# Optimization experiments

Hardware: AMD Instinct MI355X
Metric: run time of the kernel (lower is better)

Reference implementation:

```python
import jax, jax.numpy as jnp
import numpy as np

EPS = 1e-5

def _rmsnorm(x):
    # BitLinear applies a (non-learnable) RMSNorm to activations before quantization
    return x * jax.lax.rsqrt(jnp.mean(x * x, axis=-1, keepdims=True) + EPS)

def _activation_quant(x):
    # per-token absmax int8 quantization, dequantized back to float
    scale = 127.0 / jnp.clip(jnp.max(jnp.abs(x), axis=-1, keepdims=True), EPS, None)
    return jnp.clip(jnp.round(x * scale), -128, 127) / scale

def _weight_quant(w):
    # absmean ternary {-1,0,1} quantization, dequantized back to float
    scale = 1.0 / jnp.clip(jnp.mean(jnp.abs(w)), EPS, None)
    return jnp.clip(jnp.round(w * scale), -1, 1) / scale

def _bitlinear(x, w):
    xn = _rmsnorm(x)
    # straight-through estimators (identity grads through quantizers)
    xq = xn + jax.lax.stop_gradient(_activation_quant(xn) - xn)
    wq = w + jax.lax.stop_gradient(_weight_quant(w) - w)
    return jnp.einsum('bsd,hd->bsh', xq, wq)

def setup_inputs() -> dict:
    key = jax.random.key(0)
    k1, k2, k3, k4 = jax.random.split(key, 4)
    B, S, D, H = 4, 2048, 4096, 11008
    return {
        'x': jax.random.normal(k1, (B, S, D), dtype=jnp.float32),
        'w_gate': jax.random.normal(k2, (H, D), dtype=jnp.float32) * 0.02,
        'w_up': jax.random.normal(k3, (H, D), dtype=jnp.float32) * 0.02,
        'w_down': jax.random.normal(k4, (D, H), dtype=jnp.float32) * 0.02,
    }

def reference(x, w_gate, w_up, w_down):
    h = jax.nn.silu(_bitlinear(x, w_gate)) * _bitlinear(x, w_up)
    return _bitlinear(h, w_down)
```

## Files before the change

### kernel.cpp

```cpp
#include <hip/hip_runtime.h>
#include <hip/hip_bf16.h>
#include <cstdint>

#define EPS 1e-5

typedef __attribute__((ext_vector_type(4))) int int32x4;


__device__ inline float np_leaf_abs(const float* __restrict__ a, int n) {
  float r[8];
  #pragma unroll
  for (int j = 0; j < 8; j++) r[j] = fabsf(a[j]);
  for (int i = 8; i < n; i += 8) {
    #pragma unroll
    for (int j = 0; j < 8; j++) r[j] += fabsf(a[i + j]);
  }
  return ((r[0] + r[1]) + (r[2] + r[3])) + ((r[4] + r[5]) + (r[6] + r[7]));
}

__global__ __launch_bounds__(256) void np_blocksums3(
    const float* __restrict__ w0, const float* __restrict__ w1,
    const float* __restrict__ w2, float* __restrict__ bs) {
  int b = blockIdx.x * 256 + threadIdx.x;
  const float* w = (b < 131072) ? w0 : (b < 262144 ? w1 : w2);
  long lb = b & 131071;
  const float* a = w + lb * 344;
  float s0 = np_leaf_abs(a, 80);
  float s1 = np_leaf_abs(a + 80, 88);
  float s2 = np_leaf_abs(a + 168, 88);
  float s3 = np_leaf_abs(a + 256, 88);
  bs[b] = (s0 + s1) + (s2 + s3);
}

__global__ __launch_bounds__(256) void np_tree_partial3(
    const float* __restrict__ bs, float* __restrict__ part) {
  __shared__ float sh[256];
  int t = threadIdx.x;
  const float* a = bs + (long)blockIdx.x * 512;
  sh[t] = a[2 * t] + a[2 * t + 1];
  __syncthreads();
  for (int n = 128; n >= 1; n >>= 1) {
    float x = 0.f;
    if (t < n) x = sh[2 * t] + sh[2 * t + 1];
    __syncthreads();
    if (t < n) sh[t] = x;
    __syncthreads();
  }
  if (t == 0) part[blockIdx.x] = sh[0];
}

__global__ __launch_bounds__(128) void np_tree_final3(
    const float* __restrict__ part, float* __restrict__ meanw) {
  __shared__ float sh[128];
  int t = threadIdx.x;
  const float* p = part + blockIdx.x * 256;
  sh[t] = p[2 * t] + p[2 * t + 1];
  __syncthreads();
  for (int n = 64; n >= 1; n >>= 1) {
    float x = 0.f;
    if (t < n) x = sh[2 * t] + sh[2 * t + 1];
    __syncthreads();
    if (t < n) sh[t] = x;
    __syncthreads();
  }
  if (t == 0) meanw[blockIdx.x] = sh[0] / 45088768.0f;
}

__global__ __launch_bounds__(256) void quant_w_gu(
    const float* __restrict__ wg, const float* __restrict__ wu,
    const float* __restrict__ meanw, char* __restrict__ qg, char* __restrict__ qu,
    long n4) {
  int half = (blockIdx.x >= 4096);
  const float* w = half ? wu : wg;
  char* q = half ? qu : qg;
  float scale = 1.0f / fmaxf(meanw[half], 1e-5f);
  long i = (long)(blockIdx.x & 4095) * blockDim.x + threadIdx.x;
  long stride = 4096L * blockDim.x;
  const float4* w4 = (const float4*)w;
  for (; i < n4; i += stride) {
    float4 v = w4[i];
    char4 c;
    c.x = (char)(int)fminf(1.f, fmaxf(-1.f, rintf(v.x * scale)));
    c.y = (char)(int)fminf(1.f, fmaxf(-1.f, rintf(v.y * scale)));
    c.z = (char)(int)fminf(1.f, fmaxf(-1.f, rintf(v.z * scale)));
    c.w = (char)(int)fminf(1.f, fmaxf(-1.f, rintf(v.w * scale)));
    long row = i >> 10;
    int  col = (int)(i & 1023) << 2;
    long p = row >> 4; int rl = (int)(row & 15);
    int  cc = col >> 6, s = (col >> 4) & 3, j = col & 15;
    *(char4*)(q + ((p * 64 + cc) * 64 + (s << 4) + rl) * 16 + j) = c;
  }
}

#define CORR_MAX 1024
#define WIN 1e-6f

__global__ __launch_bounds__(256) void quant_w_down(
    const float* __restrict__ w, const float* __restrict__ mean_ptr,
    char* __restrict__ q, int* __restrict__ cnt,
    int* __restrict__ ck, float* __restrict__ cv) {
  float scale = 1.0f / fmaxf(mean_ptr[2], 1e-5f);
  long i0 = (long)blockIdx.x * blockDim.x + threadIdx.x;
  long stride = (long)gridDim.x * blockDim.x;
  const long ncell = 4096L * 2752L;
  for (long i = i0; i < ncell; i += stride) {
    long row = i / 2752;
    int  col = (int)(i - row * 2752) << 2;
    const float* wp = w + row * 11008 + col;
    char4 c;
    #pragma unroll
    for (int j = 0; j < 4; j++) {
      float t = wp[j] * scale;
      float qv = fminf(1.f, fmaxf(-1.f, rintf(t)));
      if (fabsf(fabsf(t) - 0.5f) < WIN) {
        qv = 0.f;
        int idx = atomicAdd(cnt, 1);
        if (idx < CORR_MAX) {
          ck[idx] = (int)(row * 11008 + col + j);
          cv[idx] = t > 0.f ? 0.5f : -0.5f;
        }
      }
      ((char*)&c)[j] = (char)(int)qv;
    }
    long p = row >> 4; int rl = (int)(row & 15);
    int  cc = col >> 6, s = (col >> 4) & 3, j = col & 15;
    *(char4*)(q + ((p * 172 + cc) * 64 + (s << 4) + rl) * 16 + j) = c;
  }
}

__global__ void zero_cnt(int* cnt) { *cnt = 0; }

__global__ __launch_bounds__(64) void apply_corr(
    const int* __restrict__ cnt, const int* __restrict__ ck,
    const float* __restrict__ cv, const char* __restrict__ qh,
    const float* __restrict__ fh, const float* __restrict__ meanw,
    float* __restrict__ out) {
  int r = blockIdx.x * 64 + threadIdx.x;
  float fwd = fmaxf(meanw[2], 1e-5f);
  int n = *cnt; if (n > CORR_MAX) n = CORR_MAX;
  float fr = fh[r] * fwd;
  long pbase = (long)(r >> 4) * 172;
  int  rl = r & 15;
  for (int i = 0; i < n; i++) {
    int flat = ck[i];
    int nn = flat / 11008, kk = flat % 11008;
    long off = ((pbase + (kk >> 6)) * 64 + (((kk >> 4) & 3) << 4) + rl) * 16 + (kk & 15);
    float qv = (float)qh[off];
    out[(long)r * 4096 + nn] += cv[i] * qv * fr;
  }
}

__device__ inline void block_reduce_sum_max_d(double& s, float& m) {
  #pragma unroll
  for (int off = 1; off < 64; off <<= 1) {
    s += __shfl_xor(s, off, 64);
    m = fmaxf(m, __shfl_xor(m, off, 64));
  }
  __shared__ double ssh[4];
  __shared__ float msh[4];
  int wv = threadIdx.x >> 6;
  if ((threadIdx.x & 63) == 0) { ssh[wv] = s; msh[wv] = m; }
  __syncthreads();
  s = (ssh[0] + ssh[1]) + (ssh[2] + ssh[3]);
  m = fmaxf(fmaxf(msh[0], msh[1]), fmaxf(msh[2], msh[3]));
}

__device__ inline char quant1d(float x, double rn, double s) {
  double t = (double)x * rn;
  double q = rint(t * s);
  q = fmin(127.0, fmax(-128.0, q));
  return (char)(int)q;
}

__global__ __launch_bounds__(256) void act_quant_x(
    const float* __restrict__ x, char* __restrict__ qx, float* __restrict__ fx) {
  __shared__ char qrow[4096];
  const int row = blockIdx.x;
  const float4* xr = (const float4*)(x + (long)row * 4096);
  float4 v[4];
  double ss = 0.0;
  float am = 0.f;
  #pragma unroll
  for (int i = 0; i < 4; i++) {
    v[i] = xr[i * 256 + threadIdx.x];
    ss += ((double)v[i].x * v[i].x + (double)v[i].y * v[i].y) +
          ((double)v[i].z * v[i].z + (double)v[i].w * v[i].w);
    am = fmaxf(am, fmaxf(fmaxf(fabsf(v[i].x), fabsf(v[i].y)),
                         fmaxf(fabsf(v[i].z), fabsf(v[i].w))));
  }
  block_reduce_sum_max_d(ss, am);
  double rn = 1.0 / sqrt(ss / 4096.0 + EPS);
  double den = fmax((double)am * rn, EPS);
  double s = 127.0 / den;
  if (threadIdx.x == 0) fx[row] = (float)(den / 127.0);
  #pragma unroll
  for (int i = 0; i < 4; i++) {
    char4 c;
    c.x = quant1d(v[i].x, rn, s);
    c.y = quant1d(v[i].y, rn, s);
    c.z = quant1d(v[i].z, rn, s);
    c.w = quant1d(v[i].w, rn, s);
    ((char4*)qrow)[i * 256 + threadIdx.x] = c;
  }
  __syncthreads();
  const int t = threadIdx.x;
  long p = row >> 4; int rl = row & 15;
  int32x4 cell = *(const int32x4*)(qrow + t * 16);
  *(int32x4*)(qx + ((p * 64 + (t >> 2)) * 64 + ((t & 3) << 4) + rl) * 16) = cell;
}

__global__ __launch_bounds__(256) void act_quant_h(
    const float* __restrict__ h, char* __restrict__ qh, float* __restrict__ fh) {
  __shared__ float4 hrow4[2752];
  __shared__ char qrow[11008];
  const long row = blockIdx.x;
  const float4* hr = (const float4*)(h + row * 11008);
  double ss = 0.0;
  float am = 0.f;
  for (int i = threadIdx.x; i < 2752; i += 256) {
    float4 v = hr[i];
    hrow4[i] = v;
    ss += ((double)v.x * v.x + (double)v.y * v.y) +
          ((double)v.z * v.z + (double)v.w * v.w);
    am = fmaxf(am, fmaxf(fmaxf(fabsf(v.x), fabsf(v.y)),
                         fmaxf(fabsf(v.z), fabsf(v.w))));
  }
  block_reduce_sum_max_d(ss, am);
  double rn = 1.0 / sqrt(ss / 11008.0 + EPS);
  double den = fmax((double)am * rn, EPS);
  double s = 127.0 / den;
  if (threadIdx.x == 0) fh[row] = (float)(den / 127.0);
  for (int i = threadIdx.x; i < 2752; i += 256) {
    float4 v = hrow4[i];
    char4 c;
    c.x = quant1d(v.x, rn, s);
    c.y = quant1d(v.y, rn, s);
    c.z = quant1d(v.z, rn, s);
    c.w = quant1d(v.w, rn, s);
    ((char4*)qrow)[i] = c;
  }
  __syncthreads();
  long p = row >> 4; int rl = (int)(row & 15);
  for (int e = threadIdx.x; e < 688; e += 256) {
    int32x4 cell = *(const int32x4*)(qrow + e * 16);
    *(int32x4*)(qh + ((p * 172 + (e >> 2)) * 64 + ((e & 3) << 4) + rl) * 16) = cell;
  }
}


__global__ __launch_bounds__(256, 2) void gemm_gateup(
    const char* __restrict__ qx, const char* __restrict__ qwg, const char* __restrict__ qwu,
    const float* __restrict__ meanw, const float* __restrict__ fx, float* __restrict__ h) {
  const int t = threadIdx.x;
  const int lane = t & 63;
  const int wv = t >> 6;
  const int bid = blockIdx.x;
  const int swz = (bid & 7) * 688 + (bid >> 3);
  const int m0 = (swz & 63) * 128;
  const int n0 = (swz >> 6) * 128;
  const int wm = (wv >> 1) * 64;
  const int wn = (wv & 1) * 64;

  const char* pA = qx  + ((long)((m0 + wm) >> 4) * 64) * 1024 + lane * 16;
  const char* pG = qwg + ((long)((n0 + wn) >> 4) * 64) * 1024 + lane * 16;
  const char* pU = qwu + ((long)((n0 + wn) >> 4) * 64) * 1024 + lane * 16;

  int32x4 accg[4][4] = {};
  int32x4 accu[4][4] = {};
  int32x4 a0[4], g0[4], u0[4], a1[4], g1[4], u1[4];

  #define GU_LOAD(ar, gr, ur, ks)                                        \
    do {                                                                 \
      _Pragma("unroll")                                                  \
      for (int m = 0; m < 4; m++)                                        \
        ar[m] = *(const int32x4*)(pA + (long)(m * 64 + (ks)) * 1024);    \
      _Pragma("unroll")                                                  \
      for (int n = 0; n < 4; n++) {                                      \
        gr[n] = *(const int32x4*)(pG + (long)(n * 64 + (ks)) * 1024);    \
        ur[n] = *(const int32x4*)(pU + (long)(n * 64 + (ks)) * 1024);    \
      }                                                                  \
    } while (0)

  #define GU_MFMA(ar, gr, ur)                                                \
    do {                                                                     \
      __builtin_amdgcn_s_setprio(1);                                         \
      _Pragma("unroll")                                                      \
      for (int n = 0; n < 4; n++) {                                          \
        _Pragma("unroll")                                                    \
        for (int m = 0; m < 4; m++) {                                        \
          accg[m][n] = __builtin_amdgcn_mfma_i32_16x16x64_i8(ar[m], gr[n], accg[m][n], 0, 0, 0); \
          accu[m][n] = __builtin_amdgcn_mfma_i32_16x16x64_i8(ar[m], ur[n], accu[m][n], 0, 0, 0); \
        }                                                                    \
      }                                                                      \
      __builtin_amdgcn_s_setprio(0);                                         \
    } while (0)

  GU_LOAD(a0, g0, u0, 0);
  for (int ks = 0; ks < 64; ks += 2) {
    if (ks + 1 < 64) GU_LOAD(a1, g1, u1, ks + 1);
    GU_MFMA(a0, g0, u0);
    if (ks + 2 < 64) GU_LOAD(a0, g0, u0, ks + 2);
    GU_MFMA(a1, g1, u1);
  }
  #undef GU_LOAD
  #undef GU_MFMA

  float fwg = fmaxf(meanw[0], 1e-5f);
  float fwu = fmaxf(meanw[1], 1e-5f);
  const int rgrp = lane >> 4;
  const int cidx = lane & 15;
  #pragma unroll
  for (int m = 0; m < 4; m++) {
    #pragma unroll
    for (int r = 0; r < 4; r++) {
      int grow = m0 + wm + m * 16 + rgrp * 4 + r;
      float fxr = fx[grow];
      float sg = fxr * fwg, su = fxr * fwu;
      #pragma unroll
      for (int n = 0; n < 4; n++) {
        float g = (float)accg[m][n][r] * sg;
        float u = (float)accu[m][n][r] * su;
        float hv = g / (1.f + expf(-g)) * u;
        h[(long)grow * 11008 + (n0 + wn + n * 16 + cidx)] = hv;
      }
    }
  }
}

__global__ __launch_bounds__(256, 2) void gemm_down(
    const char* __restrict__ qh, const char* __restrict__ qwd,
    const float* __restrict__ meanw, const float* __restrict__ fh,
    float* __restrict__ out) {
  const int t = threadIdx.x;
  const int lane = t & 63;
  const int wv = t >> 6;
  const int bid = blockIdx.x;
  const int swz = (bid & 7) * 128 + (bid >> 3);
  const int m0 = (swz & 63) * 128;
  const int n0 = (swz >> 6) * 256;
  const int wm = (wv >> 1) * 64;
  const int wn = (wv & 1) * 128;

  const char* pA = qh  + ((long)((m0 + wm) >> 4) * 172) * 1024 + lane * 16;
  const char* pB = qwd + ((long)((n0 + wn) >> 4) * 172) * 1024 + lane * 16;

  int32x4 acc[4][8] = {};
  int32x4 a0[4], b0[8], a1[4], b1[8];

  #define DN_LOAD(ar, br, ks)                                            \
    do {                                                                 \
      _Pragma("unroll")                                                  \
      for (int m = 0; m < 4; m++)                                        \
        ar[m] = *(const int32x4*)(pA + (long)(m * 172 + (ks)) * 1024);   \
      _Pragma("unroll")                                                  \
      for (int n = 0; n < 8; n++)                                        \
        br[n] = *(const int32x4*)(pB + (long)(n * 172 + (ks)) * 1024);   \
    } while (0)

  #define DN_MFMA(ar, br)                                                    \
    do {                                                                     \
      __builtin_amdgcn_s_setprio(1);                                         \
      _Pragma("unroll")                                                      \
      for (int n = 0; n < 8; n++) {                                          \
        _Pragma("unroll")                                                    \
        for (int m = 0; m < 4; m++)                                          \
          acc[m][n] = __builtin_amdgcn_mfma_i32_16x16x64_i8(ar[m], br[n], acc[m][n], 0, 0, 0); \
      }                                                                      \
      __builtin_amdgcn_s_setprio(0);                                         \
    } while (0)

  DN_LOAD(a0, b0, 0);
  for (int ks = 0; ks < 172; ks += 2) {
    if (ks + 1 < 172) DN_LOAD(a1, b1, ks + 1);
    DN_MFMA(a0, b0);
    if (ks + 2 < 172) DN_LOAD(a0, b0, ks + 2);
    DN_MFMA(a1, b1);
  }
  #undef DN_LOAD
  #undef DN_MFMA

  float fwd = fmaxf(meanw[2], 1e-5f);
  const int rgrp = lane >> 4;
  const int cidx = lane & 15;
  #pragma unroll
  for (int m = 0; m < 4; m++) {
    #pragma unroll
    for (int r = 0; r < 4; r++) {
      int grow = m0 + wm + m * 16 + rgrp * 4 + r;
      float f = fh[grow] * fwd;
      #pragma unroll
      for (int n = 0; n < 8; n++) {
        out[(long)grow * 4096 + (n0 + wn + n * 16 + cidx)] =
            (float)acc[m][n][r] * f;
      }
    }
  }
}

extern "C" void kernel_launch(void* const* d_in, const int* in_sizes, int n_in,
                              void* d_out, int out_size, void* d_ws, size_t ws_size,
                              hipStream_t stream) {
  const float* x      = (const float*)d_in[0];
  const float* w_gate = (const float*)d_in[1];
  const float* w_up   = (const float*)d_in[2];
  const float* w_down = (const float*)d_in[3];
  float* out = (float*)d_out;

  const long NW = 11008L * 4096L;
  const long NX = 8192L * 4096L;
  const long NH = 8192L * 11008L;

  char* ws  = (char*)d_ws;
  char* qwg = ws;
  char* qwu = qwg + NW;
  char* qwd = qwu + NW;
  char* qx  = qwd + NW;
  char* qh  = qx + NX;
  float* h  = (float*)(qh + NH);
  float* fx = h + NH;
  float* fh = fx + 8192;
  float* meanw = fh + 8192;
  float* bs    = meanw + 4;
  float* part  = bs + 3 * 131072;
  int*   ccnt  = (int*)(part + 1024);
  int*   ck    = ccnt + 4;
  float* cv    = (float*)(ck + CORR_MAX);

  zero_cnt<<<1, 1, 0, stream>>>(ccnt);

  np_blocksums3<<<1536, 256, 0, stream>>>(w_gate, w_up, w_down, bs);
  np_tree_partial3<<<768, 256, 0, stream>>>(bs, part);
  np_tree_final3<<<3, 128, 0, stream>>>(part, meanw);

  quant_w_gu<<<8192, 256, 0, stream>>>(w_gate, w_up, meanw, qwg, qwu, NW / 4);
  quant_w_down<<<4096, 256, 0, stream>>>(w_down, meanw, qwd, ccnt, ck, cv);

  act_quant_x<<<8192, 256, 0, stream>>>(x, qx, fx);

  gemm_gateup<<<5504, 256, 0, stream>>>(qx, qwg, qwu, meanw, fx, h);

  act_quant_h<<<8192, 256, 0, stream>>>(h, qh, fh);

  gemm_down<<<1024, 256, 0, stream>>>(qh, qwd, meanw, fh, out);

  apply_corr<<<128, 64, 0, stream>>>(ccnt, ck, cv, qh, fh, meanw, out);
}
```

Before: 1.776 ms.

## Shrink per-wave GEMM tiles and drop register double-buffering to raise occupancy

The gate/up GEMM now uses 512-thread blocks of 8 waves, each computing a 64x32 sub-tile. The down GEMM halves its block N-tile to 128 and launches twice as many blocks. Both kernels drop the explicit two-stage register prefetch for a simple single-stage loop, and launch bounds now allow 4 blocks per CU. The aim is to cut register pressure and hide memory latency through more resident waves instead of software pipelining. The cost is less data reuse per wave, so each MFMA needs more global/L2 loads, and loads are no longer overlapped explicitly.

```diff
diff --git a/kernel.cpp b/kernel.cpp
--- a/kernel.cpp
+++ b/kernel.cpp
@@ -248,7 +248,7 @@
 }
 
 
-__global__ __launch_bounds__(256, 2) void gemm_gateup(
+__global__ __launch_bounds__(512, 4) void gemm_gateup(
     const char* __restrict__ qx, const char* __restrict__ qwg, const char* __restrict__ qwu,
     const float* __restrict__ meanw, const float* __restrict__ fx, float* __restrict__ h) {
   const int t = threadIdx.x;
@@ -258,52 +258,37 @@
   const int swz = (bid & 7) * 688 + (bid >> 3);
   const int m0 = (swz & 63) * 128;
   const int n0 = (swz >> 6) * 128;
-  const int wm = (wv >> 1) * 64;
-  const int wn = (wv & 1) * 64;
+  const int wm = (wv >> 2) * 64;
+  const int wn = (wv & 3) * 32;
 
   const char* pA = qx  + ((long)((m0 + wm) >> 4) * 64) * 1024 + lane * 16;
   const char* pG = qwg + ((long)((n0 + wn) >> 4) * 64) * 1024 + lane * 16;
   const char* pU = qwu + ((long)((n0 + wn) >> 4) * 64) * 1024 + lane * 16;
 
-  int32x4 accg[4][4] = {};
-  int32x4 accu[4][4] = {};
-  int32x4 a0[4], g0[4], u0[4], a1[4], g1[4], u1[4];
-
-  #define GU_LOAD(ar, gr, ur, ks)                                        \
-    do {                                                                 \
-      _Pragma("unroll")                                                  \
-      for (int m = 0; m < 4; m++)                                        \
-        ar[m] = *(const int32x4*)(pA + (long)(m * 64 + (ks)) * 1024);    \
-      _Pragma("unroll")                                                  \
-      for (int n = 0; n < 4; n++) {                                      \
-        gr[n] = *(const int32x4*)(pG + (long)(n * 64 + (ks)) * 1024);    \
-        ur[n] = *(const int32x4*)(pU + (long)(n * 64 + (ks)) * 1024);    \
-      }                                                                  \
-    } while (0)
-
-  #define GU_MFMA(ar, gr, ur)                                                \
-    do {                                                                     \
-      __builtin_amdgcn_s_setprio(1);                                         \
-      _Pragma("unroll")                                                      \
-      for (int n = 0; n < 4; n++) {                                          \
-        _Pragma("unroll")                                                    \
-        for (int m = 0; m < 4; m++) {                                        \
-          accg[m][n] = __builtin_amdgcn_mfma_i32_16x16x64_i8(ar[m], gr[n], accg[m][n], 0, 0, 0); \
-          accu[m][n] = __builtin_amdgcn_mfma_i32_16x16x64_i8(ar[m], ur[n], accu[m][n], 0, 0, 0); \
-        }                                                                    \
-      }                                                                      \
-      __builtin_amdgcn_s_setprio(0);                                         \
-    } while (0)
-
-  GU_LOAD(a0, g0, u0, 0);
-  for (int ks = 0; ks < 64; ks += 2) {
-    if (ks + 1 < 64) GU_LOAD(a1, g1, u1, ks + 1);
-    GU_MFMA(a0, g0, u0);
-    if (ks + 2 < 64) GU_LOAD(a0, g0, u0, ks + 2);
-    GU_MFMA(a1, g1, u1);
-  }
-  #undef GU_LOAD
-  #undef GU_MFMA
+  int32x4 accg[4][2] = {};
+  int32x4 accu[4][2] = {};
+
+  for (int ks = 0; ks < 64; ++ks) {
+    int32x4 a[4], g[2], u[2];
+    #pragma unroll
+    for (int m = 0; m < 4; m++)
+      a[m] = *(const int32x4*)(pA + (long)(m * 64 + ks) * 1024);
+    #pragma unroll
+    for (int n = 0; n < 2; n++) {
+      g[n] = *(const int32x4*)(pG + (long)(n * 64 + ks) * 1024);
+      u[n] = *(const int32x4*)(pU + (long)(n * 64 + ks) * 1024);
+    }
+    __builtin_amdgcn_s_setprio(1);
+    #pragma unroll
+    for (int n = 0; n < 2; n++) {
+      #pragma unroll
+      for (int m = 0; m < 4; m++) {
+        accg[m][n] = __builtin_amdgcn_mfma_i32_16x16x64_i8(a[m], g[n], accg[m][n], 0, 0, 0);
+        accu[m][n] = __builtin_amdgcn_mfma_i32_16x16x64_i8(a[m], u[n], accu[m][n], 0, 0, 0);
+      }
+    }
+    __builtin_amdgcn_s_setprio(0);
+  }
 
   float fwg = fmaxf(meanw[0], 1e-5f);
   float fwu = fmaxf(meanw[1], 1e-5f);
@@ -317,7 +302,7 @@
       float fxr = fx[grow];
       float sg = fxr * fwg, su = fxr * fwu;
       #pragma unroll
-      for (int n = 0; n < 4; n++) {
+      for (int n = 0; n < 2; n++) {
         float g = (float)accg[m][n][r] * sg;
         float u = (float)accu[m][n][r] * su;
         float hv = g / (1.f + expf(-g)) * u;
@@ -327,7 +312,7 @@
   }
 }
 
-__global__ __launch_bounds__(256, 2) void gemm_down(
+__global__ __launch_bounds__(256, 4) void gemm_down(
     const char* __restrict__ qh, const char* __restrict__ qwd,
     const float* __restrict__ meanw, const float* __restrict__ fh,
     float* __restrict__ out) {
@@ -335,49 +320,34 @@
   const int lane = t & 63;
   const int wv = t >> 6;
   const int bid = blockIdx.x;
-  const int swz = (bid & 7) * 128 + (bid >> 3);
+  const int swz = (bid & 7) * 256 + (bid >> 3);
   const int m0 = (swz & 63) * 128;
-  const int n0 = (swz >> 6) * 256;
+  const int n0 = (swz >> 6) * 128;
   const int wm = (wv >> 1) * 64;
-  const int wn = (wv & 1) * 128;
+  const int wn = (wv & 1) * 64;
 
   const char* pA = qh  + ((long)((m0 + wm) >> 4) * 172) * 1024 + lane * 16;
   const char* pB = qwd + ((long)((n0 + wn) >> 4) * 172) * 1024 + lane * 16;
 
-  int32x4 acc[4][8] = {};
-  int32x4 a0[4], b0[8], a1[4], b1[8];
-
-  #define DN_LOAD(ar, br, ks)                                            \
-    do {                                                                 \
-      _Pragma("unroll")                                                  \
-      for (int m = 0; m < 4; m++)                                        \
-        ar[m] = *(const int32x4*)(pA + (long)(m * 172 + (ks)) * 1024);   \
-      _Pragma("unroll")                                                  \
-      for (int n = 0; n < 8; n++)                                        \
-        br[n] = *(const int32x4*)(pB + (long)(n * 172 + (ks)) * 1024);   \
-    } while (0)
-
-  #define DN_MFMA(ar, br)                                                    \
-    do {                                                                     \
-      __builtin_amdgcn_s_setprio(1);                                         \
-      _Pragma("unroll")                                                      \
-      for (int n = 0; n < 8; n++) {                                          \
-        _Pragma("unroll")                                                    \
-        for (int m = 0; m < 4; m++)                                          \
-          acc[m][n] = __builtin_amdgcn_mfma_i32_16x16x64_i8(ar[m], br[n], acc[m][n], 0, 0, 0); \
-      }                                                                      \
-      __builtin_amdgcn_s_setprio(0);                                         \
-    } while (0)
-
-  DN_LOAD(a0, b0, 0);
-  for (int ks = 0; ks < 172; ks += 2) {
-    if (ks + 1 < 172) DN_LOAD(a1, b1, ks + 1);
-    DN_MFMA(a0, b0);
-    if (ks + 2 < 172) DN_LOAD(a0, b0, ks + 2);
-    DN_MFMA(a1, b1);
-  }
-  #undef DN_LOAD
-  #undef DN_MFMA
+  int32x4 acc[4][4] = {};
+
+  for (int ks = 0; ks < 172; ++ks) {
+    int32x4 a[4], b[4];
+    #pragma unroll
+    for (int m = 0; m < 4; m++)
+      a[m] = *(const int32x4*)(pA + (long)(m * 172 + ks) * 1024);
+    #pragma unroll
+    for (int n = 0; n < 4; n++)
+      b[n] = *(const int32x4*)(pB + (long)(n * 172 + ks) * 1024);
+    __builtin_amdgcn_s_setprio(1);
+    #pragma unroll
+    for (int n = 0; n < 4; n++) {
+      #pragma unroll
+      for (int m = 0; m < 4; m++)
+        acc[m][n] = __builtin_amdgcn_mfma_i32_16x16x64_i8(a[m], b[n], acc[m][n], 0, 0, 0);
+    }
+    __builtin_amdgcn_s_setprio(0);
+  }
 
   float fwd = fmaxf(meanw[2], 1e-5f);
   const int rgrp = lane >> 4;
@@ -389,7 +359,7 @@
       int grow = m0 + wm + m * 16 + rgrp * 4 + r;
       float f = fh[grow] * fwd;
       #pragma unroll
-      for (int n = 0; n < 8; n++) {
+      for (int n = 0; n < 4; n++) {
         out[(long)grow * 4096 + (n0 + wn + n * 16 + cidx)] =
             (float)acc[m][n][r] * f;
       }
@@ -437,11 +407,11 @@
 
   act_quant_x<<<8192, 256, 0, stream>>>(x, qx, fx);
 
-  gemm_gateup<<<5504, 256, 0, stream>>>(qx, qwg, qwu, meanw, fx, h);
+  gemm_gateup<<<5504, 512, 0, stream>>>(qx, qwg, qwu, meanw, fx, h);
 
   act_quant_h<<<8192, 256, 0, stream>>>(h, qh, fh);
 
-  gemm_down<<<1024, 256, 0, stream>>>(qh, qwd, meanw, fh, out);
+  gemm_down<<<2048, 256, 0, stream>>>(qh, qwd, meanw, fh, out);
 
   apply_corr<<<128, 64, 0, stream>>>(ccnt, ck, cv, qh, fh, meanw, out);
 }
```

Result: slower. 2.119 ms (+19.3%).
